# Performance work log

Measured on AMD Instinct MI355X. Metric: run time of the kernel, lower is better.

## Reference

```python
import jax, jax.numpy as jnp
import numpy as np

TAU = 1.0
BASE = 7
NUM_TWISTS = 3
EPS = 1e-6

B, S, D, P, M = 4, 2048, 1024, 9, 256


def _rot(y, theta):
    # learned rotation in the (0,1) channel plane; theta broadcasts against y[..., 0]
    c, s = jnp.cos(theta), jnp.sin(theta)
    y0, y1 = y[..., 0], y[..., 1]
    r0 = (y0 * c - y1 * s)[..., None]
    r1 = (y0 * s + y1 * c)[..., None]
    return jnp.concatenate([r0, r1, y[..., 2:]], axis=-1)


def _mod_phase_norm(x, g, base=BASE):
    # RMS-normalize within channel groups defined by (channel index mod base)
    d = x.shape[-1]
    gid = jnp.arange(d) % base
    oh = jax.nn.one_hot(gid, base, dtype=x.dtype)           # [d, base]
    cnt = oh.sum(axis=0)                                    # [base]
    msq = (x * x) @ oh / cnt                                # [..., base]
    denom = jnp.sqrt(jnp.take(msq, gid, axis=-1) + EPS)     # [..., d]
    return x / denom * g


def setup_inputs() -> dict:
    key = jax.random.key(0)
    ks = jax.random.split(key, 16)
    w = lambda k, shape, scale: jax.random.normal(k, shape, dtype=jnp.float32) * scale
    u = jax.random.uniform(ks[1], (NUM_TWISTS + 1, B, S, P), dtype=jnp.float32,
                           minval=1e-6, maxval=1.0 - 1e-6)
    gumbel_noise = -jnp.log(-jnp.log(u))
    return {
        'x': w(ks[0], (B, S, D), 1.0),
        'gumbel_noise': gumbel_noise,
        'mixer_w': w(ks[2], (3, D), 0.5),
        'obs_W1': w(ks[3], (2 * D, M), (2 * D) ** -0.5),
        'obs_b1': jnp.zeros((M,), jnp.float32),
        'obs_th1': w(ks[4], (), 0.1),
        'obs_W2': w(ks[5], (M, P), M ** -0.5),
        'obs_b2': jnp.zeros((P,), jnp.float32),
        'obs_th2': w(ks[6], (), 0.1),
        'path_Wa': w(ks[7], (P, D, M), D ** -0.5),
        'path_ba': jnp.zeros((P, M), jnp.float32),
        'path_tha': w(ks[8], (P,), 0.1),
        'path_Wb': w(ks[9], (P, M, D), M ** -0.5),
        'path_bb': jnp.zeros((P, D), jnp.float32),
        'path_thb': w(ks[10], (P,), 0.1),
        'twist_W': w(ks[11], (D, D), D ** -0.5),
        'twist_b': jnp.zeros((D,), jnp.float32),
        'twist_th': w(ks[12], (), 0.1),
        'norm_g': jnp.ones((D,), jnp.float32),
    }


def reference(x, gumbel_noise, mixer_w, obs_W1, obs_b1, obs_th1, obs_W2, obs_b2,
              obs_th2, path_Wa, path_ba, path_tha, path_Wb, path_bb, path_thb,
              twist_W, twist_b, twist_th, norm_g):
    # neighbor mixer: per-channel 3-tap mix over sequence (zero-padded, non-causal)
    xp = jnp.pad(x, ((0, 0), (1, 1), (0, 0)))
    x_mixed = x * mixer_w[0] + xp[:, :-2] * mixer_w[1] + xp[:, 2:] * mixer_w[2]

    def observer_logits(collapsed):
        combined = jnp.concatenate([x_mixed, collapsed], axis=-1)      # [B,S,2D]
        h = jnp.tanh(_rot(combined @ obs_W1 + obs_b1, obs_th1))        # [B,S,M]
        return _rot(h @ obs_W2 + obs_b2, obs_th2)                      # [B,S,P]

    def path_outputs_fn(tin):
        h = _rot(jnp.einsum('bsd,pdm->bspm', tin, path_Wa) + path_ba, path_tha)
        return _rot(jnp.einsum('bspm,pmd->bspd', h, path_Wb) + path_bb, path_thb)

    collapsed = jnp.zeros_like(x_mixed)
    path_out = None
    for t in range(NUM_TWISTS):
        logits = observer_logits(collapsed)
        rw = jax.nn.softmax((logits + gumbel_noise[t]) / TAU, axis=-1)  # soft gumbel
        tin = x_mixed + _rot(collapsed @ twist_W + twist_b, twist_th)
        path_out = path_outputs_fn(tin)                                # [B,S,P,D]
        collapsed = _mod_phase_norm(jnp.einsum('bspd,bsp->bsd', path_out, rw), norm_g)

    # final hard (straight-through) gumbel routing, reusing last path_out
    final_logits = observer_logits(collapsed)
    soft = jax.nn.softmax((final_logits + gumbel_noise[NUM_TWISTS]) / TAU, axis=-1)
    hard = jax.nn.one_hot(jnp.argmax(soft, axis=-1), P, dtype=soft.dtype)
    rw_hard = hard + soft - jax.lax.stop_gradient(soft)
    final_collapsed = jnp.einsum('bspd,bsp->bsd', path_out, rw_hard)

    # dropout is identity in eval mode
    out = _mod_phase_norm(x + final_collapsed, norm_g)
    collapsed = _mod_phase_norm(collapsed, norm_g)
    return out, collapsed
```

## Files before the change

kernel.cpp:

```cpp
#include <hip/hip_runtime.h>
#include <hip/hip_bf16.h>

typedef unsigned short u16;
typedef short bf16x8 __attribute__((ext_vector_type(8)));
typedef float f32x4 __attribute__((ext_vector_type(4)));

constexpr int Dd = 1024, Pp = 9, Mm = 256, Nn = 8192, Kc = 2304;
constexpr float EPSf = 1e-6f;

__device__ __forceinline__ float bf2f(u16 u) {
    union { unsigned int u; float f; } v; v.u = ((unsigned int)u) << 16; return v.f;
}
__device__ __forceinline__ u16 f2bf(float f) {
    union { float f; unsigned int u; } v; v.f = f;
    unsigned int r = (v.u + 0x7FFFu + ((v.u >> 16) & 1u)) >> 16; return (u16)r;
}
__device__ __forceinline__ void split2(float v, u16& h, u16& l) {
    h = f2bf(v); l = f2bf(v - bf2f(h));
}
__device__ __forceinline__ void gld16(u16* lds, const u16* g) {
    __builtin_amdgcn_global_load_lds(
        (const __attribute__((address_space(1))) unsigned int*)g,
        (__attribute__((address_space(3))) unsigned int*)lds, 16, 0, 0);
}

__global__ void rotcopy_k(const float* __restrict__ src, float* __restrict__ dst,
                          int R, int C, const float* __restrict__ theta, int Pb)
{
    long total = (long)Pb * R * C;
    long idx = (long)blockIdx.x * 256 + threadIdx.x;
    if (idx >= total) return;
    int c = (int)(idx % C);
    long rp = idx / C;
    int r = (int)(rp % R);
    int pb = (int)(rp / R);
    float th = theta[pb];
    const float* s = src + ((long)pb * R + r) * C;
    float v;
    if (c == 0)      v = s[0] * cosf(th) - s[1] * sinf(th);
    else if (c == 1) v = s[0] * sinf(th) + s[1] * cosf(th);
    else             v = s[c];
    dst[idx] = v;
}

__global__ void splitW1_k(const float* __restrict__ W1, const float* __restrict__ th,
                          u16* __restrict__ h, u16* __restrict__ l)
{
    int idx = blockIdx.x * 256 + threadIdx.x;
    if (idx >= 256 * 2048) return;
    int k = idx & 2047, n = idx >> 11;
    float v;
    if (n == 0)      v = W1[(long)k * 256 + 0] * cosf(th[0]) - W1[(long)k * 256 + 1] * sinf(th[0]);
    else if (n == 1) v = W1[(long)k * 256 + 0] * sinf(th[0]) + W1[(long)k * 256 + 1] * cosf(th[0]);
    else             v = W1[(long)k * 256 + n];
    u16 hh, ll; split2(v, hh, ll); h[idx] = hh; l[idx] = ll;
}

__global__ void splitTW_k(const float* __restrict__ tW, const float* __restrict__ th,
                          u16* __restrict__ h, u16* __restrict__ l)
{
    int idx = blockIdx.x * 256 + threadIdx.x;
    if (idx >= 1024 * 1024) return;
    int k = idx & 1023, n = idx >> 10;
    float v;
    if (n == 0)      v = tW[(long)k * 1024 + 0] * cosf(th[0]) - tW[(long)k * 1024 + 1] * sinf(th[0]);
    else if (n == 1) v = tW[(long)k * 1024 + 0] * sinf(th[0]) + tW[(long)k * 1024 + 1] * cosf(th[0]);
    else             v = tW[(long)k * 1024 + n];
    u16 hh, ll; split2(v, hh, ll); h[idx] = hh; l[idx] = ll;
}

__global__ void splitWa_k(const float* __restrict__ Wa, const float* __restrict__ tha,
                          u16* __restrict__ h, u16* __restrict__ l)
{
    int idx = blockIdx.x * 256 + threadIdx.x;
    if (idx >= Kc * 1024) return;
    int k = idx & 1023, n = idx >> 10;
    int p = n >> 8, m = n & 255;
    const float* s = Wa + ((long)p * 1024 + k) * 256;
    float v;
    if (m == 0)      v = s[0] * cosf(tha[p]) - s[1] * sinf(tha[p]);
    else if (m == 1) v = s[0] * sinf(tha[p]) + s[1] * cosf(tha[p]);
    else             v = s[m];
    u16 hh, ll; split2(v, hh, ll); h[idx] = hh; l[idx] = ll;
}

__global__ void splitWb_k(const float* __restrict__ Wb, const float* __restrict__ thb,
                          u16* __restrict__ h, u16* __restrict__ l)
{
    int idx = blockIdx.x * 256 + threadIdx.x;
    if (idx >= 1024 * Kc) return;
    int n = idx / Kc;
    int k = idx - n * Kc;
    int p = k >> 8, m = k & 255;
    const float* s = Wb + ((long)p * 256 + m) * 1024;
    float v;
    if (n == 0)      v = s[0] * cosf(thb[p]) - s[1] * sinf(thb[p]);
    else if (n == 1) v = s[0] * sinf(thb[p]) + s[1] * cosf(thb[p]);
    else             v = s[n];
    u16 hh, ll; split2(v, hh, ll); h[idx] = hh; l[idx] = ll;
}

__global__ void mixer_k(const float* __restrict__ x, const float* __restrict__ mw,
                        u16* __restrict__ xmh, u16* __restrict__ xml)
{
    int idx = blockIdx.x * 256 + threadIdx.x;
    if (idx >= Nn * Dd / 4) return;
    int d4 = idx & (Dd / 4 - 1);
    int n = idx >> 8;
    int s = n & 2047;
    const float4* x4 = (const float4*)x;
    const float4* w4 = (const float4*)mw;
    float4 xc = x4[idx];
    float4 w0 = w4[d4], w1 = w4[(Dd / 4) + d4], w2 = w4[2 * (Dd / 4) + d4];
    float o[4];
    o[0] = xc.x * w0.x; o[1] = xc.y * w0.y; o[2] = xc.z * w0.z; o[3] = xc.w * w0.w;
    if (s > 0) {
        float4 xl = x4[idx - Dd / 4];
        o[0] += xl.x * w1.x; o[1] += xl.y * w1.y; o[2] += xl.z * w1.z; o[3] += xl.w * w1.w;
    }
    if (s < 2047) {
        float4 xr = x4[idx + Dd / 4];
        o[0] += xr.x * w2.x; o[1] += xr.y * w2.y; o[2] += xr.z * w2.z; o[3] += xr.w * w2.w;
    }
    ushort4 h4, l4;
    split2(o[0], h4.x, l4.x); split2(o[1], h4.y, l4.y);
    split2(o[2], h4.z, l4.z); split2(o[3], h4.w, l4.w);
    ((ushort4*)xmh)[idx] = h4; ((ushort4*)xml)[idx] = l4;
}

__global__ void tanh_k(const float* __restrict__ a, float* __restrict__ o, int total)
{
    int idx = blockIdx.x * 256 + threadIdx.x;
    if (idx < total) o[idx] = tanhf(a[idx]);
}

__global__ void addb_split_k(const u16* __restrict__ xmh, const u16* __restrict__ xml,
                             const float* __restrict__ tbr,
                             u16* __restrict__ th_, u16* __restrict__ tl_)
{
    int idx = blockIdx.x * 256 + threadIdx.x;
    if (idx >= Nn * Dd / 4) return;
    int d4 = idx & (Dd / 4 - 1);
    ushort4 xh = ((const ushort4*)xmh)[idx], xl = ((const ushort4*)xml)[idx];
    float4 b = ((const float4*)tbr)[d4];
    ushort4 h4, l4;
    split2(bf2f(xh.x) + bf2f(xl.x) + b.x, h4.x, l4.x);
    split2(bf2f(xh.y) + bf2f(xl.y) + b.y, h4.y, l4.y);
    split2(bf2f(xh.z) + bf2f(xl.z) + b.z, h4.z, l4.z);
    split2(bf2f(xh.w) + bf2f(xl.w) + b.w, h4.w, l4.w);
    ((ushort4*)th_)[idx] = h4; ((ushort4*)tl_)[idx] = l4;
}

template<int EPI>
__global__ __launch_bounds__(256, 2) void mgemm(
    const u16* __restrict__ Agh, const u16* __restrict__ Agl, int lda,
    const u16* __restrict__ Bgh, const u16* __restrict__ Bgl, int ldb,
    int K,
    float* __restrict__ Cf, int ldc,
    const float* __restrict__ Cinit,
    const float* __restrict__ bias,
    const float* __restrict__ rwv,
    const float* __restrict__ rwv2,
    const float* __restrict__ bbrv)
{
    __shared__ u16 smem[2][16384];
    const int tid = threadIdx.x, wave = tid >> 6, lane = tid & 63;
    const int nwg = gridDim.x * gridDim.y;
    const int flat = blockIdx.y * gridDim.x + blockIdx.x;
    const int q = nwg >> 3;
    const int l_ = (flat & 7) * q + (flat >> 3);
    const int r0 = (l_ / gridDim.x) * 128, c0 = (l_ % gridDim.x) * 128;
    const int srl = lane >> 2;
    const int ssl = ((lane & 3) ^ ((lane >> 3) & 3)) * 8;
    const int frl = lane & 15, kh = lane >> 4;
    const int sw  = (kh ^ ((frl >> 1) & 3)) * 8;
    const int arow0 = (wave >> 1) * 64, bcol0 = (wave & 1) * 64;
    const int w32 = wave * 32;

    f32x4 acc[4][4] = {};
    f32x4 acc2[4][4];
    if constexpr (EPI == 4) {
#pragma unroll
        for (int i = 0; i < 4; ++i)
#pragma unroll
            for (int j = 0; j < 4; ++j) acc2[i][j] = f32x4{0.f, 0.f, 0.f, 0.f};
    }

    auto STAGE = [&](int buf, int k0) {
        u16* base = &smem[buf][0];
        u16* As_h = base;        u16* As_l = base + 4096;
        u16* Bs_h = base + 8192; u16* Bs_l = base + 12288;
        const long ga0 = (long)(r0 + w32 + srl) * lda + k0 + ssl;
        gld16(&As_h[w32 * 32],        Agh + ga0);
        gld16(&As_h[(w32 + 16) * 32], Agh + ga0 + 16L * lda);
        gld16(&As_l[w32 * 32],        Agl + ga0);
        gld16(&As_l[(w32 + 16) * 32], Agl + ga0 + 16L * lda);
        const long gb0 = (long)(c0 + w32 + srl) * ldb + k0 + ssl;
        gld16(&Bs_h[w32 * 32],        Bgh + gb0);
        gld16(&Bs_h[(w32 + 16) * 32], Bgh + gb0 + 16L * ldb);
        gld16(&Bs_l[w32 * 32],        Bgl + gb0);
        gld16(&Bs_l[(w32 + 16) * 32], Bgl + gb0 + 16L * ldb);
    };
    auto COMPUTE = [&](int buf, f32x4 (&ac)[4][4]) {
        u16* base = &smem[buf][0];
        u16* As_h = base;        u16* As_l = base + 4096;
        u16* Bs_h = base + 8192; u16* Bs_l = base + 12288;
        bf16x8 ah[4], al[4];
#pragma unroll
        for (int f = 0; f < 4; ++f) {
            int ao = (arow0 + f * 16 + frl) * 32 + sw;
            ah[f] = *(const bf16x8*)&As_h[ao];
            al[f] = *(const bf16x8*)&As_l[ao];
        }
#pragma unroll
        for (int j = 0; j < 4; ++j) {
            int bo = (bcol0 + j * 16 + frl) * 32 + sw;
            bf16x8 bh = *(const bf16x8*)&Bs_h[bo];
            bf16x8 bl = *(const bf16x8*)&Bs_l[bo];
#pragma unroll
            for (int i = 0; i < 4; ++i) {
                ac[i][j] = __builtin_amdgcn_mfma_f32_16x16x32_bf16(ah[i], bh, ac[i][j], 0, 0, 0);
                ac[i][j] = __builtin_amdgcn_mfma_f32_16x16x32_bf16(ah[i], bl, ac[i][j], 0, 0, 0);
                ac[i][j] = __builtin_amdgcn_mfma_f32_16x16x32_bf16(al[i], bh, ac[i][j], 0, 0, 0);
            }
        }
    };
    auto FLUSH = [&](int p) {
#pragma unroll
        for (int i = 0; i < 4; ++i)
#pragma unroll
            for (int reg = 0; reg < 4; ++reg) {
                float w = rwv[(long)(r0 + arow0 + i * 16 + kh * 4 + reg) * 9 + p];
#pragma unroll
                for (int j = 0; j < 4; ++j) {
                    acc[i][j][reg] += w * acc2[i][j][reg];
                    acc2[i][j][reg] = 0.f;
                }
            }
    };

    const int NT = K / 32;
    STAGE(0, 0);
#pragma unroll 1
    for (int t = 0; t < NT; t += 2) {
        STAGE(1, (t + 1) * 32);
        asm volatile("s_waitcnt vmcnt(8)" ::: "memory");
        __builtin_amdgcn_sched_barrier(0);
        __builtin_amdgcn_s_barrier();
        __builtin_amdgcn_sched_barrier(0);
        if constexpr (EPI == 4) COMPUTE(0, acc2); else COMPUTE(0, acc);
        __builtin_amdgcn_sched_barrier(0);
        __builtin_amdgcn_s_barrier();
        __builtin_amdgcn_sched_barrier(0);
        if (t + 2 < NT) {
            STAGE(0, (t + 2) * 32);
            asm volatile("s_waitcnt vmcnt(8)" ::: "memory");
        } else {
            asm volatile("s_waitcnt vmcnt(0)" ::: "memory");
        }
        __builtin_amdgcn_sched_barrier(0);
        __builtin_amdgcn_s_barrier();
        __builtin_amdgcn_sched_barrier(0);
        if constexpr (EPI == 4) COMPUTE(1, acc2); else COMPUTE(1, acc);
        __builtin_amdgcn_sched_barrier(0);
        __builtin_amdgcn_s_barrier();
        __builtin_amdgcn_sched_barrier(0);
        if constexpr (EPI == 4) {
            if (((t + 1) & 7) == 7) FLUSH((t + 1) >> 3);
        }
    }

#pragma unroll
    for (int i = 0; i < 4; ++i)
#pragma unroll
        for (int reg = 0; reg < 4; ++reg) {
            const int r = r0 + arow0 + i * 16 + kh * 4 + reg;
#pragma unroll
            for (int j = 0; j < 4; ++j) {
                const int c = c0 + bcol0 + j * 16 + frl;
                float v = acc[i][j][reg];
                if constexpr (EPI == 0) {
                    Cf[(long)r * ldc + c] = v + bias[c];
                } else if constexpr (EPI == 1) {
                    Cf[(long)r * ldc + c] = tanhf(v + Cinit[(long)r * ldc + c]);
                } else if constexpr (EPI == 4) {
#pragma unroll
                    for (int p = 0; p < 9; ++p) v += rwv2[(long)r * 9 + p] * bbrv[p * 1024 + c];
                    Cf[(long)r * ldc + c] = v;
                }
            }
        }
}

template<int EPI>
__global__ __launch_bounds__(512, 2) void mgemm3(
    const u16* __restrict__ Agh, const u16* __restrict__ Agl, int lda,
    const u16* __restrict__ Bgh, const u16* __restrict__ Bgl, int ldb,
    int K,
    float* __restrict__ Cf, u16* __restrict__ Coh, u16* __restrict__ Col, int ldc,
    const u16* __restrict__ CIh, const u16* __restrict__ CIl,
    const float* __restrict__ bias,
    const float* __restrict__ rwv,
    const float* __restrict__ bbrv)
{
    __shared__ u16 smem[2][24576];
    const int tid = threadIdx.x, wave = tid >> 6, lane = tid & 63;
    const int nwg = gridDim.x * gridDim.y;
    const int flat = blockIdx.y * gridDim.x + blockIdx.x;
    const int q = nwg >> 3;
    const int l_ = (flat & 7) * q + (flat >> 3);
    const int r0 = (l_ / gridDim.x) * 256, c0 = (l_ % gridDim.x) * 128;
    const int srl = lane >> 2;
    const int ssl = ((lane & 3) ^ ((lane >> 3) & 3)) * 8;
    const int frl = lane & 15, kh = lane >> 4;
    const int sw  = (kh ^ ((frl >> 1) & 3)) * 8;
    const int arow0 = (wave >> 1) * 64, bcol0 = (wave & 1) * 64;
    const int w32 = wave * 32, w16 = wave * 16;
    const int NT = K / 32;

    f32x4 acc[4][4] = {};

    auto STAGE = [&](int buf, int k0) {
        u16* Ash = &smem[buf][0];
        u16* Asl = &smem[buf][8192];
        u16* Bsh = &smem[buf][16384];
        u16* Bsl = &smem[buf][20480];
        const long ga = (long)(r0 + w32 + srl) * lda + k0 + ssl;
        gld16(&Ash[w32 * 32],        Agh + ga);
        gld16(&Ash[(w32 + 16) * 32], Agh + ga + 16L * lda);
        gld16(&Asl[w32 * 32],        Agl + ga);
        gld16(&Asl[(w32 + 16) * 32], Agl + ga + 16L * lda);
        const long gb = (long)(c0 + w16 + srl) * ldb + k0 + ssl;
        gld16(&Bsh[w16 * 32], Bgh + gb);
        gld16(&Bsl[w16 * 32], Bgl + gb);
    };
    auto COMPUTE = [&](int buf) {
        const u16* Ash = &smem[buf][0];
        const u16* Asl = &smem[buf][8192];
        const u16* Bsh = &smem[buf][16384];
        const u16* Bsl = &smem[buf][20480];
        bf16x8 ah[4], al[4], bh[4], bl[4];
#pragma unroll
        for (int f = 0; f < 4; ++f) {
            int ao = (arow0 + f * 16 + frl) * 32 + sw;
            ah[f] = *(const bf16x8*)&Ash[ao];
            al[f] = *(const bf16x8*)&Asl[ao];
            int bo = (bcol0 + f * 16 + frl) * 32 + sw;
            bh[f] = *(const bf16x8*)&Bsh[bo];
            bl[f] = *(const bf16x8*)&Bsl[bo];
        }
        __builtin_amdgcn_s_setprio(1);
#pragma unroll
        for (int j = 0; j < 4; ++j)
#pragma unroll
            for (int i = 0; i < 4; ++i) {
                acc[i][j] = __builtin_amdgcn_mfma_f32_16x16x32_bf16(ah[i], bh[j], acc[i][j], 0, 0, 0);
                acc[i][j] = __builtin_amdgcn_mfma_f32_16x16x32_bf16(ah[i], bl[j], acc[i][j], 0, 0, 0);
                acc[i][j] = __builtin_amdgcn_mfma_f32_16x16x32_bf16(al[i], bh[j], acc[i][j], 0, 0, 0);
            }
        __builtin_amdgcn_s_setprio(0);
    };

    STAGE(0, 0);
    asm volatile("s_waitcnt vmcnt(0)" ::: "memory");
    __builtin_amdgcn_sched_barrier(0);
    __builtin_amdgcn_s_barrier();
    __builtin_amdgcn_sched_barrier(0);

#pragma unroll 1
    for (int t = 0; t < NT; t += 2) {
        STAGE(1, (t + 1) * 32);
        COMPUTE(0);
        asm volatile("s_waitcnt vmcnt(0)" ::: "memory");
        __builtin_amdgcn_sched_barrier(0);
        __builtin_amdgcn_s_barrier();
        __builtin_amdgcn_sched_barrier(0);
        if (t + 2 < NT) STAGE(0, (t + 2) * 32);
        COMPUTE(1);
        asm volatile("s_waitcnt vmcnt(0)" ::: "memory");
        __builtin_amdgcn_sched_barrier(0);
        __builtin_amdgcn_s_barrier();
        __builtin_amdgcn_sched_barrier(0);
    }

#pragma unroll
    for (int i = 0; i < 4; ++i)
#pragma unroll
        for (int reg = 0; reg < 4; ++reg) {
            const int r = r0 + arow0 + i * 16 + kh * 4 + reg;
#pragma unroll
            for (int j = 0; j < 4; ++j) {
                const int c = c0 + bcol0 + j * 16 + frl;
                float v = acc[i][j][reg];
                if constexpr (EPI == 2) {
                    long o = (long)r * ldc + c;
                    v += bf2f(CIh[o]) + bf2f(CIl[o]) + bias[c];
                    u16 h, l; split2(v, h, l); Coh[o] = h; Col[o] = l;
                } else if constexpr (EPI == 3) {
                    long o = (long)r * ldc + c;
                    v = (v + bias[c]) * rwv[(long)r * 9 + (c >> 8)];
                    u16 h, l; split2(v, h, l); Coh[o] = h; Col[o] = l;
                } else {
#pragma unroll
                    for (int p = 0; p < 9; ++p) v += rwv[(long)r * 9 + p] * bbrv[p * 1024 + c];
                    Cf[(long)r * ldc + c] = v;
                }
            }
        }
}

__global__ void logits_k(const float* __restrict__ h, const float* __restrict__ W2r,
                         const float* __restrict__ b2r, const float* __restrict__ gum,
                         float* __restrict__ rwA, float* __restrict__ rwH,
                         const float* __restrict__ rwS, int hard)
{
    __shared__ float hs[Mm];
    __shared__ float lg[16];
    int n = blockIdx.x;
    for (int i = threadIdx.x; i < Mm; i += 64) hs[i] = h[(long)n * Mm + i];
    __syncthreads();
    if (threadIdx.x < Pp) {
        int p = threadIdx.x;
        float acc = b2r[p];
        for (int m = 0; m < Mm; ++m) acc += hs[m] * W2r[m * Pp + p];
        lg[p] = acc + gum[(long)n * Pp + p];
    }
    __syncthreads();
    if (threadIdx.x == 0) {
        float mx = lg[0]; int am = 0;
#pragma unroll
        for (int p = 1; p < Pp; ++p) if (lg[p] > mx) { mx = lg[p]; am = p; }
        if (hard) {
#pragma unroll
            for (int p = 0; p < Pp; ++p) {
                rwA[(long)n * Pp + p] = (p == am) ? 1.f / rwS[(long)n * Pp + p] : 0.f;
                rwH[(long)n * Pp + p] = (p == am) ? 1.f : 0.f;
            }
        } else {
            float e[Pp]; float ssum = 0.f;
#pragma unroll
            for (int p = 0; p < Pp; ++p) { e[p] = expf(lg[p] - mx); ssum += e[p]; }
#pragma unroll
            for (int p = 0; p < Pp; ++p) rwA[(long)n * Pp + p] = e[p] / ssum;
        }
    }
}

template<int INSPLIT, int OUTSPLIT>
__global__ void norm_k(const float* __restrict__ in,
                       const u16* __restrict__ inh, const u16* __restrict__ inl,
                       const float* __restrict__ add, const float* __restrict__ g,
                       float* __restrict__ outf, u16* __restrict__ oh, u16* __restrict__ ol)
{
    __shared__ float sb[256][8];
    __shared__ float dn[8];
    int n = blockIdx.x;
    int t = threadIdx.x;
    float v[4];
#pragma unroll
    for (int j = 0; j < 7; ++j) sb[t][j] = 0.f;
#pragma unroll
    for (int i = 0; i < 4; ++i) {
        int d = t + i * 256;
        long o = (long)n * Dd + d;
        float xv = INSPLIT ? (bf2f(inh[o]) + bf2f(inl[o])) : in[o];
        if (add) xv += add[o];
        v[i] = xv;
        sb[t][d % 7] += xv * xv;
    }
    __syncthreads();
    for (int st = 128; st >= 1; st >>= 1) {
        if (t < st) {
#pragma unroll
            for (int j = 0; j < 7; ++j) sb[t][j] += sb[t + st][j];
        }
        __syncthreads();
    }
    if (t < 7) {
        const float cnt = (t < 2) ? 147.f : 146.f;
        dn[t] = 1.f / sqrtf(sb[0][t] / cnt + EPSf);
    }
    __syncthreads();
#pragma unroll
    for (int i = 0; i < 4; ++i) {
        int d = t + i * 256;
        long o = (long)n * Dd + d;
        float ov = v[i] * dn[d % 7] * g[d];
        if (OUTSPLIT) { u16 h, l; split2(ov, h, l); oh[o] = h; ol[o] = l; }
        else outf[o] = ov;
    }
}

static inline int cdiv(long a, long b) { return (int)((a + b - 1) / b); }

extern "C" void kernel_launch(void* const* d_in, const int* in_sizes, int n_in,
                              void* d_out, int out_size, void* d_ws, size_t ws_size,
                              hipStream_t stream)
{
    const float* x    = (const float*)d_in[0];
    const float* gum  = (const float*)d_in[1];
    const float* mw   = (const float*)d_in[2];
    const float* W1   = (const float*)d_in[3];
    const float* b1   = (const float*)d_in[4];
    const float* th1  = (const float*)d_in[5];
    const float* W2   = (const float*)d_in[6];
    const float* b2   = (const float*)d_in[7];
    const float* th2  = (const float*)d_in[8];
    const float* Wa   = (const float*)d_in[9];
    const float* ba   = (const float*)d_in[10];
    const float* tha  = (const float*)d_in[11];
    const float* Wb   = (const float*)d_in[12];
    const float* bbv  = (const float*)d_in[13];
    const float* thb  = (const float*)d_in[14];
    const float* tW   = (const float*)d_in[15];
    const float* tb   = (const float*)d_in[16];
    const float* tth  = (const float*)d_in[17];
    const float* gnorm = (const float*)d_in[18];

    char* cur = (char*)d_ws;
    auto alloc = [&](size_t bytes) -> void* {
        void* r = (void*)cur; cur += (bytes + 255) & ~(size_t)255; return r;
    };
    void* region = alloc((size_t)Nn * Dd * 4);
    float* craw = (float*)region;
    float* hbuf = (float*)region;
    u16*   tinh = (u16*)region;
    u16*   tinl = tinh + (size_t)Nn * Dd;
    float* zx   = (float*)alloc((size_t)Nn * Mm * 4);
    float* rwS  = (float*)alloc((size_t)Nn * Pp * 4);
    float* rwD  = (float*)alloc((size_t)Nn * Pp * 4);
    float* rwH  = (float*)alloc((size_t)Nn * Pp * 4);
    u16* xmh  = (u16*)alloc((size_t)Nn * Dd * 2);
    u16* xml  = (u16*)alloc((size_t)Nn * Dd * 2);
    u16* colh = (u16*)alloc((size_t)Nn * Dd * 2);
    u16* coll = (u16*)alloc((size_t)Nn * Dd * 2);
    u16* hph  = (u16*)alloc((size_t)Nn * Kc * 2);
    u16* hpl  = (u16*)alloc((size_t)Nn * Kc * 2);
    u16* W1th = (u16*)alloc(256 * 2048 * 2);
    u16* W1tl = (u16*)alloc(256 * 2048 * 2);
    u16* tWth = (u16*)alloc(1024 * 1024 * 2);
    u16* tWtl = (u16*)alloc(1024 * 1024 * 2);
    u16* Wath = (u16*)alloc((size_t)Kc * 1024 * 2);
    u16* Watl = (u16*)alloc((size_t)Kc * 1024 * 2);
    u16* Wbth = (u16*)alloc((size_t)1024 * Kc * 2);
    u16* Wbtl = (u16*)alloc((size_t)1024 * Kc * 2);
    float* W2r = (float*)alloc(256 * 9 * 4);
    float* b1r = (float*)alloc(256 * 4);
    float* b2r = (float*)alloc(16 * 4);
    float* bac = (float*)alloc(Kc * 4);
    float* bbr = (float*)alloc(Pp * 1024 * 4);
    float* tbr = (float*)alloc(1024 * 4);
    if ((size_t)(cur - (char*)d_ws) > ws_size) return;

    float* out0 = (float*)d_out;
    float* out1 = out0 + (long)Nn * Dd;

    splitW1_k<<<2048, 256, 0, stream>>>(W1, th1, W1th, W1tl);
    splitTW_k<<<4096, 256, 0, stream>>>(tW, tth, tWth, tWtl);
    splitWa_k<<<cdiv((long)Kc * 1024, 256), 256, 0, stream>>>(Wa, tha, Wath, Watl);
    splitWb_k<<<cdiv((long)1024 * Kc, 256), 256, 0, stream>>>(Wb, thb, Wbth, Wbtl);
    rotcopy_k<<<cdiv(256L * 9, 256), 256, 0, stream>>>(W2, W2r, 256, 9, th2, 1);
    rotcopy_k<<<1, 256, 0, stream>>>(b1, b1r, 1, 256, th1, 1);
    rotcopy_k<<<1, 256, 0, stream>>>(b2, b2r, 1, 9, th2, 1);
    rotcopy_k<<<cdiv((long)Pp * Mm, 256), 256, 0, stream>>>(ba, bac, 1, 256, tha, 9);
    rotcopy_k<<<cdiv((long)Pp * 1024, 256), 256, 0, stream>>>(bbv, bbr, 1, 1024, thb, 9);
    rotcopy_k<<<cdiv(1024L, 256), 256, 0, stream>>>(tb, tbr, 1, 1024, tth, 1);

    mixer_k<<<Nn * Dd / 4 / 256, 256, 0, stream>>>(x, mw, xmh, xml);

    mgemm<0><<<dim3(2, 64), 256, 0, stream>>>(
        xmh, xml, 1024, W1th, W1tl, 2048, 1024,
        zx, 256, nullptr, b1r, nullptr, nullptr, nullptr);

    for (int t = 0; t < 3; ++t) {
        if (t == 0) {
            tanh_k<<<cdiv((long)Nn * Mm, 256), 256, 0, stream>>>(zx, hbuf, Nn * Mm);
        } else {
            mgemm<1><<<dim3(2, 64), 256, 0, stream>>>(
                colh, coll, 1024, W1th + 1024, W1tl + 1024, 2048, 1024,
                hbuf, 256, zx, nullptr, nullptr, nullptr, nullptr);
        }
        logits_k<<<Nn, 64, 0, stream>>>(hbuf, W2r, b2r, gum + (long)t * Nn * Pp,
                                        rwS, nullptr, nullptr, 0);
        if (t == 0) {
            addb_split_k<<<Nn * Dd / 4 / 256, 256, 0, stream>>>(xmh, xml, tbr, tinh, tinl);
        } else {
            mgemm3<2><<<dim3(8, 32), 512, 0, stream>>>(
                colh, coll, 1024, tWth, tWtl, 1024, 1024,
                nullptr, tinh, tinl, 1024, xmh, xml, tbr, nullptr, nullptr);
        }
        mgemm3<3><<<dim3(18, 32), 512, 0, stream>>>(
            tinh, tinl, 1024, Wath, Watl, 1024, 1024,
            nullptr, hph, hpl, Kc, nullptr, nullptr, bac, rwS, nullptr);
        mgemm3<5><<<dim3(8, 32), 512, 0, stream>>>(
            hph, hpl, Kc, Wbth, Wbtl, Kc, Kc,
            craw, nullptr, nullptr, 1024, nullptr, nullptr, nullptr, rwS, bbr);
        norm_k<0, 1><<<Nn, 256, 0, stream>>>(craw, nullptr, nullptr, nullptr, gnorm,
                                             nullptr, colh, coll);
    }

    mgemm<1><<<dim3(2, 64), 256, 0, stream>>>(
        colh, coll, 1024, W1th + 1024, W1tl + 1024, 2048, 1024,
        hbuf, 256, zx, nullptr, nullptr, nullptr, nullptr);
    logits_k<<<Nn, 64, 0, stream>>>(hbuf, W2r, b2r, gum + 3L * Nn * Pp,
                                    rwD, rwH, rwS, 1);
    mgemm<4><<<dim3(8, 64), 256, 0, stream>>>(
        hph, hpl, Kc, Wbth, Wbtl, Kc, Kc,
        craw, 1024, nullptr, nullptr, rwD, rwH, bbr);
    norm_k<0, 0><<<Nn, 256, 0, stream>>>(craw, nullptr, nullptr, x, gnorm, out0, nullptr, nullptr);
    norm_k<1, 0><<<Nn, 256, 0, stream>>>(nullptr, colh, coll, nullptr, gnorm, out1, nullptr, nullptr);
}
```

Before: 1.415 ms.

## Triple-buffer LDS in split-bf16 GEMM to keep two tiles in flight

Replaces the double-buffered LDS pipeline in mgemm3 with a three-buffer rotating pipeline. Two K-tiles are prefetched ahead, and the kernel waits with vmcnt(6) so that only the oldest tile must have landed, using one barrier per iteration instead of two. The aim is to hide global-load latency better and cut barrier stalls. The cost is that LDS per block rises to about 147KB, which likely rules out the two blocks per CU requested by launch_bounds and lowers occupancy.

```diff
diff --git a/kernel.cpp b/kernel.cpp
--- a/kernel.cpp
+++ b/kernel.cpp
@@ -303,7 +303,7 @@
     const float* __restrict__ rwv,
     const float* __restrict__ bbrv)
 {
-    __shared__ u16 smem[2][24576];
+    __shared__ u16 smem[3 * 24576];
     const int tid = threadIdx.x, wave = tid >> 6, lane = tid & 63;
     const int nwg = gridDim.x * gridDim.y;
     const int flat = blockIdx.y * gridDim.x + blockIdx.x;
@@ -320,11 +320,11 @@
 
     f32x4 acc[4][4] = {};
 
-    auto STAGE = [&](int buf, int k0) {
-        u16* Ash = &smem[buf][0];
-        u16* Asl = &smem[buf][8192];
-        u16* Bsh = &smem[buf][16384];
-        u16* Bsl = &smem[buf][20480];
+    auto STAGE = [&](u16* base, int k0) {
+        u16* Ash = base;
+        u16* Asl = base + 8192;
+        u16* Bsh = base + 16384;
+        u16* Bsl = base + 20480;
         const long ga = (long)(r0 + w32 + srl) * lda + k0 + ssl;
         gld16(&Ash[w32 * 32],        Agh + ga);
         gld16(&Ash[(w32 + 16) * 32], Agh + ga + 16L * lda);
@@ -334,11 +334,11 @@
         gld16(&Bsh[w16 * 32], Bgh + gb);
         gld16(&Bsl[w16 * 32], Bgl + gb);
     };
-    auto COMPUTE = [&](int buf) {
-        const u16* Ash = &smem[buf][0];
-        const u16* Asl = &smem[buf][8192];
-        const u16* Bsh = &smem[buf][16384];
-        const u16* Bsl = &smem[buf][20480];
+    auto COMPUTE = [&](const u16* base) {
+        const u16* Ash = base;
+        const u16* Asl = base + 8192;
+        const u16* Bsh = base + 16384;
+        const u16* Bsl = base + 20480;
         bf16x8 ah[4], al[4], bh[4], bl[4];
 #pragma unroll
         for (int f = 0; f < 4; ++f) {
@@ -361,27 +361,23 @@
         __builtin_amdgcn_s_setprio(0);
     };
 
-    STAGE(0, 0);
-    asm volatile("s_waitcnt vmcnt(0)" ::: "memory");
+    u16* b0 = smem;
+    u16* b1 = smem + 24576;
+    u16* b2 = smem + 49152;
+    STAGE(b0, 0);
+    STAGE(b1, 32);
+#pragma unroll 1
+    for (int t = 0; t < NT; ++t) {
+        if (t + 1 < NT) asm volatile("s_waitcnt vmcnt(6)" ::: "memory");
+        else            asm volatile("s_waitcnt vmcnt(0)" ::: "memory");
+        __builtin_amdgcn_sched_barrier(0);
+        __builtin_amdgcn_s_barrier();
+        __builtin_amdgcn_sched_barrier(0);
+        if (t + 2 < NT) STAGE(b2, (t + 2) * 32);
+        COMPUTE(b0);
+        u16* tp = b0; b0 = b1; b1 = b2; b2 = tp;
+    }
     __builtin_amdgcn_sched_barrier(0);
-    __builtin_amdgcn_s_barrier();
-    __builtin_amdgcn_sched_barrier(0);
-
-#pragma unroll 1
-    for (int t = 0; t < NT; t += 2) {
-        STAGE(1, (t + 1) * 32);
-        COMPUTE(0);
-        asm volatile("s_waitcnt vmcnt(0)" ::: "memory");
-        __builtin_amdgcn_sched_barrier(0);
-        __builtin_amdgcn_s_barrier();
-        __builtin_amdgcn_sched_barrier(0);
-        if (t + 2 < NT) STAGE(0, (t + 2) * 32);
-        COMPUTE(1);
-        asm volatile("s_waitcnt vmcnt(0)" ::: "memory");
-        __builtin_amdgcn_sched_barrier(0);
-        __builtin_amdgcn_s_barrier();
-        __builtin_amdgcn_sched_barrier(0);
-    }
 
 #pragma unroll
     for (int i = 0; i < 4; ++i)
```

Measured after the change: 1.459 ms. +3.1%, slower.
